# Optimization experiments

Hardware: AMD Instinct MI355X
Metric: run time of the kernel (lower is better)

The kernel has to match this reference:

```python
import jax, jax.numpy as jnp
import numpy as np

M, N = 2048, 128  # m basis operators, n-dim Hilbert space

def setup_inputs() -> dict:
    key = jax.random.key(0)
    k1, k2, k3, k4 = jax.random.split(key, 4)
    return {
        "basis_re": jax.random.normal(k1, (M, N, N), dtype=jnp.float32),
        "basis_im": jax.random.normal(k2, (M, N, N), dtype=jnp.float32),
        "theta": jax.random.uniform(k3, (4, N), dtype=jnp.float32, minval=-1.0, maxval=1.0),
        "evl": jax.random.uniform(k4, (2,), dtype=jnp.float32, minval=-1.0, maxval=1.0),
    }

def reference(basis_re, basis_im, theta, evl):
    m = basis_re.shape[0]
    # basis_orth_conj: conj of basis, flattened to (m, n*n)
    B = (basis_re - 1j * basis_im).reshape(m, -1)
    # first eigenvector
    c0 = theta[0] + 1j * theta[1]
    evc0 = c0 / jnp.linalg.norm(c0)
    # second eigenvector, Gram-Schmidt against evc0 (vdot conjugates 1st arg)
    c1 = theta[2] + 1j * theta[3]
    c1 = c1 - jnp.vdot(evc0, c1) * evc0
    evc1 = c1 / jnp.linalg.norm(c1)
    # eigenvalues: softplus then L2-normalize
    lam = jax.nn.softplus(evl)
    lam = lam / jnp.linalg.norm(lam)
    # rank-2 Hermitian: lam0 * evc0 evc0^H - lam1 * evc1 evc1^H  (n, n)
    matH = evc0[:, None] * (evc0.conj() * lam[0]) - evc1[:, None] * (evc1.conj() * lam[1])
    # (m, n^2) @ (n^2,) complex matvec, then squared L2 norm
    v = B @ matH.reshape(-1)
    return jnp.sum((v.conj() * v).real)
```

## Files before the change

### kernel.cpp

```cpp
#include <hip/hip_runtime.h>

#define N 128
#define NN (N * N)
#define M 2048

__device__ __forceinline__ float block_reduce128(float v, float* red, int i) {
    __syncthreads();
    red[i] = v;
    __syncthreads();
    for (int off = 64; off > 0; off >>= 1) {
        if (i < off) red[i] += red[i + off];
        __syncthreads();
    }
    return red[0];
}

__global__ void prep_kernel(const float* __restrict__ theta,
                            const float* __restrict__ evl,
                            float* __restrict__ ws) {
    __shared__ float red[N];
    const int i = threadIdx.x;

    float c0r = theta[i], c0i = theta[N + i];
    float s0 = block_reduce128(c0r * c0r + c0i * c0i, red, i);
    float inv0 = rsqrtf(s0);
    float a0r = c0r * inv0, a0i = c0i * inv0;

    float c1r = theta[2 * N + i], c1i = theta[3 * N + i];
    float dr = block_reduce128(a0r * c1r + a0i * c1i, red, i);
    float di = block_reduce128(a0r * c1i - a0i * c1r, red, i);
    c1r -= dr * a0r - di * a0i;
    c1i -= dr * a0i + di * a0r;

    float s1 = block_reduce128(c1r * c1r + c1i * c1i, red, i);
    float inv1 = rsqrtf(s1);
    float a1r = c1r * inv1, a1i = c1i * inv1;

    ws[i]         = a0r;
    ws[N + i]     = a0i;
    ws[2 * N + i] = a1r;
    ws[3 * N + i] = a1i;
    if (i == 0) {
        float l0 = log1pf(expf(evl[0]));
        float l1 = log1pf(expf(evl[1]));
        float inl = rsqrtf(l0 * l0 + l1 * l1);
        ws[4 * N]     = l0 * inl;
        ws[4 * N + 1] = l1 * inl;
    }
}

#define COMP(comp)                                                   \
    {                                                                \
        float x0r = e0ri * E0r.comp + e0ii * E0i.comp;               \
        float x0i = e0ii * E0r.comp - e0ri * E0i.comp;               \
        float x1r = e1ri * E1r.comp + e1ii * E1i.comp;               \
        float x1i = e1ii * E1r.comp - e1ri * E1i.comp;               \
        float hr = lam0 * x0r - lam1 * x1r;                          \
        float hi = lam0 * x0i - lam1 * x1i;                          \
        vr += a.comp * hr + b.comp * hi;                             \
        vi += a.comp * hi - b.comp * hr;                             \
    }

__global__ __launch_bounds__(256, 8) void main_kernel(
        const float4* __restrict__ br, const float4* __restrict__ bi,
        const float* __restrict__ ws, float* __restrict__ out) {
    __shared__ __align__(16) float le[4 * N];
    __shared__ float slam[2];
    __shared__ float swr[4], swi[4];
    const int t = threadIdx.x;
    const int k = blockIdx.x;

    if (t < 128) {
        le[t]       = ws[t];
        le[t + 128] = ws[t + 128];
        le[t + 256] = ws[t + 256];
        le[t + 384] = ws[t + 384];
    }
    if (t < 2) slam[t] = ws[512 + t];
    __syncthreads();
    const float lam0 = slam[0], lam1 = slam[1];
    const float4* e0r4 = (const float4*)(le);
    const float4* e0i4 = (const float4*)(le + 128);
    const float4* e1r4 = (const float4*)(le + 256);
    const float4* e1i4 = (const float4*)(le + 384);

    const float4* brk = br + (size_t)k * (NN / 4);
    const float4* bik = bi + (size_t)k * (NN / 4);

    float vr = 0.f, vi = 0.f;
    float4 a0 = brk[t];
    float4 b0 = bik[t];
    #pragma unroll
    for (int c = 0; c < 16; ++c) {
        float4 a = a0, b = b0;
        if (c < 15) {
            a0 = brk[t + 256 * (c + 1)];
            b0 = bik[t + 256 * (c + 1)];
        }
        const int it = t + 256 * c;
        const int i  = it >> 5;
        const int j4 = it & 31;
        const float e0ri = le[i],       e0ii = le[128 + i];
        const float e1ri = le[256 + i], e1ii = le[384 + i];
        const float4 E0r = e0r4[j4], E0i = e0i4[j4];
        const float4 E1r = e1r4[j4], E1i = e1i4[j4];
        COMP(x) COMP(y) COMP(z) COMP(w)
    }

    for (int off = 32; off > 0; off >>= 1) {
        vr += __shfl_down(vr, off);
        vi += __shfl_down(vi, off);
    }
    const int wave = t >> 6, lane = t & 63;
    if (lane == 0) { swr[wave] = vr; swi[wave] = vi; }
    __syncthreads();
    if (t == 0) {
        float R = swr[0] + swr[1] + swr[2] + swr[3];
        float I = swi[0] + swi[1] + swi[2] + swi[3];
        atomicAdd(out, R * R + I * I);
    }
}

extern "C" void kernel_launch(void* const* d_in, const int* in_sizes, int n_in,
                              void* d_out, int out_size, void* d_ws, size_t ws_size,
                              hipStream_t stream) {
    const float* basis_re = (const float*)d_in[0];
    const float* basis_im = (const float*)d_in[1];
    const float* theta    = (const float*)d_in[2];
    const float* evl      = (const float*)d_in[3];
    float* out = (float*)d_out;
    float* ws  = (float*)d_ws;

    hipMemsetAsync(d_out, 0, sizeof(float), stream);
    prep_kernel<<<1, 128, 0, stream>>>(theta, evl, ws);
    main_kernel<<<M, 256, 0, stream>>>((const float4*)basis_re,
                                       (const float4*)basis_im,
                                       ws, out);
}
```

Baseline: 287.3 us.

## Factor rank-2 Hermitian into scaled eigenvectors and deepen load prefetch

Folds sqrt of the eigenvalue weights into the eigenvectors so the matvec splits into two outer-product contractions. Each thread reduces along its column block first and applies the row factor once per step, which cuts per-element FLOPs. Loads are issued earlier with a three-deep register prefetch, and global loads start before the shared-memory setup. The atomicAdd is replaced with per-block partials plus a separate reduce kernel, and the memset is dropped. This adds an extra launch and relies on both eigenvalue weights being nonnegative, which softplus guarantees.

```diff
diff --git a/kernel.cpp b/kernel.cpp
--- a/kernel.cpp
+++ b/kernel.cpp
@@ -34,78 +34,95 @@
 
     float s1 = block_reduce128(c1r * c1r + c1i * c1i, red, i);
     float inv1 = rsqrtf(s1);
-    float a1r = c1r * inv1, a1i = c1i * inv1;
 
-    ws[i]         = a0r;
-    ws[N + i]     = a0i;
-    ws[2 * N + i] = a1r;
-    ws[3 * N + i] = a1i;
-    if (i == 0) {
-        float l0 = log1pf(expf(evl[0]));
-        float l1 = log1pf(expf(evl[1]));
-        float inl = rsqrtf(l0 * l0 + l1 * l1);
-        ws[4 * N]     = l0 * inl;
-        ws[4 * N + 1] = l1 * inl;
-    }
+    float l0 = log1pf(expf(evl[0]));
+    float l1 = log1pf(expf(evl[1]));
+    float inl = rsqrtf(l0 * l0 + l1 * l1);
+    float sc0 = sqrtf(l0 * inl);
+    float sc1 = sqrtf(l1 * inl);
+
+    ws[i]         = a0r * sc0;
+    ws[N + i]     = a0i * sc0;
+    ws[2 * N + i] = c1r * inv1 * sc1;
+    ws[3 * N + i] = c1i * inv1 * sc1;
 }
 
-#define COMP(comp)                                                   \
-    {                                                                \
-        float x0r = e0ri * E0r.comp + e0ii * E0i.comp;               \
-        float x0i = e0ii * E0r.comp - e0ri * E0i.comp;               \
-        float x1r = e1ri * E1r.comp + e1ii * E1i.comp;               \
-        float x1i = e1ii * E1r.comp - e1ri * E1i.comp;               \
-        float hr = lam0 * x0r - lam1 * x1r;                          \
-        float hi = lam0 * x0i - lam1 * x1i;                          \
-        vr += a.comp * hr + b.comp * hi;                             \
-        vi += a.comp * hi - b.comp * hr;                             \
+#define ELEM(comp, A, B)                                         \
+    {                                                            \
+        a0r = fmaf((A).comp, E0r.comp, a0r);                     \
+        a0r = fmaf(-(B).comp, E0i.comp, a0r);                    \
+        a0i = fmaf(-(A).comp, E0i.comp, a0i);                    \
+        a0i = fmaf(-(B).comp, E0r.comp, a0i);                    \
+        a1r = fmaf((A).comp, E1r.comp, a1r);                     \
+        a1r = fmaf(-(B).comp, E1i.comp, a1r);                    \
+        a1i = fmaf(-(A).comp, E1i.comp, a1i);                    \
+        a1i = fmaf(-(B).comp, E1r.comp, a1i);                    \
+    }
+
+#define STEP(c, A, B)                                            \
+    {                                                            \
+        float a0r = 0.f, a0i = 0.f, a1r = 0.f, a1i = 0.f;        \
+        ELEM(x, A, B) ELEM(y, A, B) ELEM(z, A, B) ELEM(w, A, B)  \
+        const int irow = bi0 + 8 * (c);                          \
+        const float er0 = le[irow],       ei0 = le[128 + irow];  \
+        const float er1 = le[256 + irow], ei1 = le[384 + irow];  \
+        v0r = fmaf(er0, a0r, v0r); v0r = fmaf(-ei0, a0i, v0r);   \
+        v0i = fmaf(er0, a0i, v0i); v0i = fmaf(ei0, a0r, v0i);    \
+        v1r = fmaf(er1, a1r, v1r); v1r = fmaf(-ei1, a1i, v1r);   \
+        v1i = fmaf(er1, a1i, v1i); v1i = fmaf(ei1, a1r, v1i);    \
+    }
+
+#define PF(A, B, c)                                              \
+    {                                                            \
+        A = brk[t + 256 * (c)];                                  \
+        B = bik[t + 256 * (c)];                                  \
     }
 
 __global__ __launch_bounds__(256, 8) void main_kernel(
         const float4* __restrict__ br, const float4* __restrict__ bi,
-        const float* __restrict__ ws, float* __restrict__ out) {
+        const float* __restrict__ ws, float* __restrict__ partial) {
     __shared__ __align__(16) float le[4 * N];
-    __shared__ float slam[2];
     __shared__ float swr[4], swi[4];
     const int t = threadIdx.x;
     const int k = blockIdx.x;
 
-    if (t < 128) {
-        le[t]       = ws[t];
-        le[t + 128] = ws[t + 128];
-        le[t + 256] = ws[t + 256];
-        le[t + 384] = ws[t + 384];
-    }
-    if (t < 2) slam[t] = ws[512 + t];
-    __syncthreads();
-    const float lam0 = slam[0], lam1 = slam[1];
-    const float4* e0r4 = (const float4*)(le);
-    const float4* e0i4 = (const float4*)(le + 128);
-    const float4* e1r4 = (const float4*)(le + 256);
-    const float4* e1i4 = (const float4*)(le + 384);
-
     const float4* brk = br + (size_t)k * (NN / 4);
     const float4* bik = bi + (size_t)k * (NN / 4);
 
-    float vr = 0.f, vi = 0.f;
-    float4 a0 = brk[t];
-    float4 b0 = bik[t];
-    #pragma unroll
-    for (int c = 0; c < 16; ++c) {
-        float4 a = a0, b = b0;
-        if (c < 15) {
-            a0 = brk[t + 256 * (c + 1)];
-            b0 = bik[t + 256 * (c + 1)];
-        }
-        const int it = t + 256 * c;
-        const int i  = it >> 5;
-        const int j4 = it & 31;
-        const float e0ri = le[i],       e0ii = le[128 + i];
-        const float e1ri = le[256 + i], e1ii = le[384 + i];
-        const float4 E0r = e0r4[j4], E0i = e0i4[j4];
-        const float4 E1r = e1r4[j4], E1i = e1i4[j4];
-        COMP(x) COMP(y) COMP(z) COMP(w)
-    }
+    float4 A0 = brk[t],       B0 = bik[t];
+    float4 A1 = brk[t + 256], B1 = bik[t + 256];
+    float4 A2 = brk[t + 512], B2 = bik[t + 512];
+
+    if (t < 128) ((float4*)le)[t] = ((const float4*)ws)[t];
+    __syncthreads();
+
+    const int j4  = t & 31;
+    const int bi0 = t >> 5;
+    const float4* e4 = (const float4*)le;
+    const float4 E0r = e4[j4],      E0i = e4[32 + j4];
+    const float4 E1r = e4[64 + j4], E1i = e4[96 + j4];
+
+    float v0r = 0.f, v0i = 0.f, v1r = 0.f, v1i = 0.f;
+
+    STEP(0,  A0, B0) PF(A0, B0, 3)
+    STEP(1,  A1, B1) PF(A1, B1, 4)
+    STEP(2,  A2, B2) PF(A2, B2, 5)
+    STEP(3,  A0, B0) PF(A0, B0, 6)
+    STEP(4,  A1, B1) PF(A1, B1, 7)
+    STEP(5,  A2, B2) PF(A2, B2, 8)
+    STEP(6,  A0, B0) PF(A0, B0, 9)
+    STEP(7,  A1, B1) PF(A1, B1, 10)
+    STEP(8,  A2, B2) PF(A2, B2, 11)
+    STEP(9,  A0, B0) PF(A0, B0, 12)
+    STEP(10, A1, B1) PF(A1, B1, 13)
+    STEP(11, A2, B2) PF(A2, B2, 14)
+    STEP(12, A0, B0) PF(A0, B0, 15)
+    STEP(13, A1, B1)
+    STEP(14, A2, B2)
+    STEP(15, A0, B0)
+
+    float vr = v0r - v1r;
+    float vi = v0i - v1i;
 
     for (int off = 32; off > 0; off >>= 1) {
         vr += __shfl_down(vr, off);
@@ -117,8 +134,21 @@
     if (t == 0) {
         float R = swr[0] + swr[1] + swr[2] + swr[3];
         float I = swi[0] + swi[1] + swi[2] + swi[3];
-        atomicAdd(out, R * R + I * I);
+        partial[k] = R * R + I * I;
     }
+}
+
+__global__ __launch_bounds__(256) void reduce_kernel(
+        const float* __restrict__ partial, float* __restrict__ out) {
+    __shared__ float sw[4];
+    const int t = threadIdx.x;
+    float s = 0.f;
+    #pragma unroll
+    for (int r = 0; r < M / 256; ++r) s += partial[t + 256 * r];
+    for (int off = 32; off > 0; off >>= 1) s += __shfl_down(s, off);
+    if ((t & 63) == 0) sw[t >> 6] = s;
+    __syncthreads();
+    if (t == 0) out[0] = sw[0] + sw[1] + sw[2] + sw[3];
 }
 
 extern "C" void kernel_launch(void* const* d_in, const int* in_sizes, int n_in,
@@ -131,9 +161,9 @@
     float* out = (float*)d_out;
     float* ws  = (float*)d_ws;
 
-    hipMemsetAsync(d_out, 0, sizeof(float), stream);
     prep_kernel<<<1, 128, 0, stream>>>(theta, evl, ws);
     main_kernel<<<M, 256, 0, stream>>>((const float4*)basis_re,
                                        (const float4*)basis_im,
-                                       ws, out);
+                                       ws, ws + 512);
+    reduce_kernel<<<1, 256, 0, stream>>>(ws + 512, out);
 }
```

After: 288.7 us. Within noise of the previous version (+0.5%).
